# Kernel tuning notes

Measured on AMD Instinct MI355X. Metric: run time of the kernel, lower is better.

## Reference

```python
import jax, jax.numpy as jnp
import numpy as np

B, E, C, I, O, T = 8, 8, 1024, 128, 256, 8192

def setup_inputs() -> dict:
    key = jax.random.key(0)
    k1, k2, k3, k4, k5 = jax.random.split(key, 5)
    x_expert = jax.random.normal(k1, (B, E, C, I), dtype=jnp.float32)
    expert_indices = jax.random.randint(k2, (B, E, C), 0, T, dtype=jnp.int64 if jax.config.jax_enable_x64 else jnp.int32)
    expert_gate = jax.random.uniform(k3, (B, E, C), dtype=jnp.float32)
    # learned params: nn.Linear(in_features=1024, out_features=256) -> weight (O, in) viewed as (E, O, I)
    bound = 1.0 / np.sqrt(E * I)
    weight = jax.random.uniform(k4, (E, O, I), dtype=jnp.float32, minval=-bound, maxval=bound)
    bias = jax.random.uniform(k5, (O,), dtype=jnp.float32, minval=-bound, maxval=bound)
    return {"x_expert": x_expert, "expert_indices": expert_indices, "expert_gate": expert_gate,
            "weight": weight, "bias": bias, "num_tokens": T}

def reference(x_expert, expert_indices, expert_gate, weight, bias, num_tokens):
    # per-expert GEMM: (B,E,C,I) x (E,O,I) -> (B,E,C,O)
    y = jnp.einsum('beci,eoi->beco', x_expert, weight) + bias
    # gate scale: gate (B,E,C) -> (B,E,C,1)
    y = y * expert_gate[..., None]
    # scatter-add combine: flatten expert/capacity dims and index_add into (B, T, O)
    Bq, Eq, Cq, Oq = y.shape
    flat_y = y.reshape(Bq, Eq * Cq, Oq)
    flat_idx = expert_indices.reshape(Bq, Eq * Cq)
    out = jnp.zeros((Bq, num_tokens, Oq), dtype=y.dtype)
    batch_idx = jnp.arange(Bq)[:, None]  # (B,1) broadcasts against (B, E*C)
    out = out.at[batch_idx, flat_idx].add(flat_y)
    return out
```

## Files before the change

### kernel.cpp

```cpp
#include <hip/hip_runtime.h>

constexpr int Bn = 8;
constexpr int En = 8;
constexpr int Cn = 1024;
constexpr int In = 128;
constexpr int On = 256;
constexpr int Tn = 8192;
constexpr int ECn = En * Cn;

constexpr int TT = 64;

typedef __fp16 fp16x2 __attribute__((ext_vector_type(2)));
typedef __fp16 f16x8  __attribute__((ext_vector_type(8)));
typedef float  f32x4  __attribute__((ext_vector_type(4)));

__device__ inline unsigned int pk16(float a, float b) {
    fp16x2 h = __builtin_amdgcn_cvt_pkrtz(a, b);
    return __builtin_bit_cast(unsigned int, h);
}

__global__ void prep_w(const float4* __restrict__ w4, uint4* __restrict__ wh4) {
    int f = blockIdx.x * 256 + threadIdx.x;
    int col = f & 255, q = (f >> 8) & 3, s = (f >> 10) & 3, e = f >> 12;
    const float4* p = w4 + ((size_t)(e * On + col)) * (In / 4) + (s * 8 + q * 2);
    float4 a = p[0], b = p[1];
    uint4 o;
    o.x = pk16(a.x, a.y); o.y = pk16(a.z, a.w);
    o.z = pk16(b.x, b.y); o.w = pk16(b.z, b.w);
    wh4[f] = o;
}

__global__ __launch_bounds__(256, 2)
void gemm_scatter(const float* __restrict__ x,
                  const int*   __restrict__ idx,
                  const float* __restrict__ gate,
                  const uint4* __restrict__ wh4,
                  const float* __restrict__ bias,
                  float* __restrict__ out)
{
    __shared__ uint4 Ah[TT * 16];
    __shared__ int   sIdx[TT];
    __shared__ float sG[TT];

    const int tid = threadIdx.x;
    const int blk = blockIdx.x;
    const int b  = blk >> 7;
    const int e  = (blk >> 4) & 7;
    const int c0 = (blk & 15) * TT;

    const size_t becBase = ((size_t)(b * En + e)) * Cn + c0;
    const float* xrow = x + becBase * In;

    if (tid < TT) {
        sIdx[tid] = idx[becBase + tid];
        sG[tid]   = gate[becBase + tid];
    }

    {
        const int tl = tid >> 2, cq = (tid & 3) * 4;
        const float4* xr = (const float4*)xrow + (size_t)tl * (In / 4);
        #pragma unroll
        for (int it = 0; it < 4; ++it) {
            int cc = cq + it;
            float4 a = xr[2 * cc], b2 = xr[2 * cc + 1];
            uint4 o;
            o.x = pk16(a.x, a.y);  o.y = pk16(a.z, a.w);
            o.z = pk16(b2.x, b2.y); o.w = pk16(b2.z, b2.w);
            Ah[tl * 16 + (cc ^ (tl & 15))] = o;
        }
    }

    const int l15  = tid & 15;
    const int q    = (tid >> 4) & 3;
    const int wcol = (tid >> 6) * 64;

    f16x8 bfr[4][4];
    #pragma unroll
    for (int nt = 0; nt < 4; ++nt)
        #pragma unroll
        for (int s = 0; s < 4; ++s)
            bfr[nt][s] = __builtin_bit_cast(f16x8,
                wh4[(size_t)((e * 4 + s) * 4 + q) * 256 + wcol + 16 * nt + l15]);

    __syncthreads();

    f32x4 acc[4][4];
    #pragma unroll
    for (int mt = 0; mt < 4; ++mt)
        #pragma unroll
        for (int nt = 0; nt < 4; ++nt) acc[mt][nt] = f32x4{0.f, 0.f, 0.f, 0.f};

    #pragma unroll
    for (int mt = 0; mt < 4; ++mt) {
        const int tl = mt * 16 + l15;
        f16x8 afr[4];
        #pragma unroll
        for (int s = 0; s < 4; ++s)
            afr[s] = __builtin_bit_cast(f16x8, Ah[tl * 16 + ((4 * s + q) ^ (tl & 15))]);
        #pragma unroll
        for (int nt = 0; nt < 4; ++nt)
            #pragma unroll
            for (int s = 0; s < 4; ++s)
                acc[mt][nt] = __builtin_amdgcn_mfma_f32_16x16x32_f16(
                    afr[s], bfr[nt][s], acc[mt][nt], 0, 0, 0);
    }

    float bv[4];
    #pragma unroll
    for (int nt = 0; nt < 4; ++nt) bv[nt] = bias[wcol + 16 * nt + l15];

    float* ob = out + (size_t)b * Tn * On;
    #pragma unroll
    for (int mt = 0; mt < 4; ++mt) {
        #pragma unroll
        for (int i = 0; i < 4; ++i) {
            const int tl = mt * 16 + q * 4 + i;
            const int t  = sIdx[tl];
            const float g = sG[tl];
            float* orow = ob + (size_t)t * On + wcol + l15;
            #pragma unroll
            for (int nt = 0; nt < 4; ++nt)
                atomicAdd(&orow[16 * nt], (acc[mt][nt][i] + bv[nt]) * g);
        }
    }
}

extern "C" void kernel_launch(void* const* d_in, const int* in_sizes, int n_in,
                              void* d_out, int out_size, void* d_ws, size_t ws_size,
                              hipStream_t stream) {
    const float* x    = (const float*)d_in[0];
    const int*   idx  = (const int*)  d_in[1];
    const float* gate = (const float*)d_in[2];
    const float* w    = (const float*)d_in[3];
    const float* bias = (const float*)d_in[4];
    float* out = (float*)d_out;

    uint4* wh4 = (uint4*)d_ws;

    prep_w<<<(En * 4 * 4 * On) / 256, 256, 0, stream>>>((const float4*)w, wh4);
    hipMemsetAsync(d_out, 0, (size_t)out_size, stream);

    const int nblk = Bn * En * (Cn / TT);
    gemm_scatter<<<nblk, 256, 0, stream>>>(x, idx, gate, wh4, bias, out);
}
```

Before: 151.0 us.

## Replace atomic scatter with GEMM-to-workspace plus gather-based combine per token

When the workspace is large enough, the GEMM writes unscaled per-slot outputs to a workspace buffer. A second kernel then builds, per block of 64 tokens, a shared-memory inverse index of contributing slots and gathers and gates those rows, adding bias times the gate sum. This removes the global float atomics and the output memset, and the weights are converted to fp16 inside the GEMM instead of in a separate prep kernel. The cost is an extra 64 MB write and read of the workspace, and every combine block scans the whole index array. It also relies on a fixed per-token capacity plus a small overflow list, so tokens with very many contributions could be dropped.

```diff
diff --git a/kernel.cpp b/kernel.cpp
--- a/kernel.cpp
+++ b/kernel.cpp
@@ -8,7 +8,9 @@
 constexpr int Tn = 8192;
 constexpr int ECn = En * Cn;
 
-constexpr int TT = 64;
+constexpr int TT  = 64;
+constexpr int CAP = 16;
+constexpr int OVF = 32;
 
 typedef __fp16 fp16x2 __attribute__((ext_vector_type(2)));
 typedef __fp16 f16x8  __attribute__((ext_vector_type(8)));
@@ -17,6 +19,194 @@
 __device__ inline unsigned int pk16(float a, float b) {
     fp16x2 h = __builtin_amdgcn_cvt_pkrtz(a, b);
     return __builtin_bit_cast(unsigned int, h);
+}
+
+__global__ __launch_bounds__(256, 2)
+void gemm_y(const float* __restrict__ x,
+            const float* __restrict__ w,
+            float* __restrict__ y)
+{
+    __shared__ uint4 Ah[TT * 16];
+
+    const int tid = threadIdx.x;
+    const int blk = blockIdx.x;
+    const int b  = blk >> 7;
+    const int e  = (blk >> 4) & 7;
+    const int c0 = (blk & 15) * TT;
+
+    const size_t becBase = ((size_t)(b * En + e)) * Cn + c0;
+    const float* xrow = x + becBase * In;
+
+    {
+        const int tl = tid >> 2, cq = (tid & 3) * 4;
+        const float4* xr = (const float4*)xrow + (size_t)tl * (In / 4);
+        #pragma unroll
+        for (int it = 0; it < 4; ++it) {
+            int cc = cq + it;
+            float4 a = xr[2 * cc], b2 = xr[2 * cc + 1];
+            uint4 o;
+            o.x = pk16(a.x, a.y);   o.y = pk16(a.z, a.w);
+            o.z = pk16(b2.x, b2.y); o.w = pk16(b2.z, b2.w);
+            Ah[tl * 16 + (cc ^ (tl & 15))] = o;
+        }
+    }
+
+    const int l15  = tid & 15;
+    const int q    = (tid >> 4) & 3;
+    const int wcol = (tid >> 6) * 64;
+
+    f16x8 bfr[4][4];
+    #pragma unroll
+    for (int nt = 0; nt < 4; ++nt)
+        #pragma unroll
+        for (int s = 0; s < 4; ++s) {
+            const int col = wcol + 16 * nt + l15;
+            const float4* p = (const float4*)w
+                + ((size_t)(e * On + col)) * (In / 4) + (s * 8 + q * 2);
+            float4 a = p[0], b2 = p[1];
+            uint4 o;
+            o.x = pk16(a.x, a.y);   o.y = pk16(a.z, a.w);
+            o.z = pk16(b2.x, b2.y); o.w = pk16(b2.z, b2.w);
+            bfr[nt][s] = __builtin_bit_cast(f16x8, o);
+        }
+
+    __syncthreads();
+
+    f32x4 acc[4][4];
+    #pragma unroll
+    for (int mt = 0; mt < 4; ++mt)
+        #pragma unroll
+        for (int nt = 0; nt < 4; ++nt) acc[mt][nt] = f32x4{0.f, 0.f, 0.f, 0.f};
+
+    #pragma unroll
+    for (int mt = 0; mt < 4; ++mt) {
+        const int tl = mt * 16 + l15;
+        f16x8 afr[4];
+        #pragma unroll
+        for (int s = 0; s < 4; ++s)
+            afr[s] = __builtin_bit_cast(f16x8, Ah[tl * 16 + ((4 * s + q) ^ (tl & 15))]);
+        #pragma unroll
+        for (int nt = 0; nt < 4; ++nt)
+            #pragma unroll
+            for (int s = 0; s < 4; ++s)
+                acc[mt][nt] = __builtin_amdgcn_mfma_f32_16x16x32_f16(
+                    afr[s], bfr[nt][s], acc[mt][nt], 0, 0, 0);
+    }
+
+    float* yb = y + becBase * On;
+    #pragma unroll
+    for (int mt = 0; mt < 4; ++mt) {
+        #pragma unroll
+        for (int i = 0; i < 4; ++i) {
+            const int tl = mt * 16 + q * 4 + i;
+            float* yr = yb + (size_t)tl * On + wcol + l15;
+            #pragma unroll
+            for (int nt = 0; nt < 4; ++nt)
+                yr[16 * nt] = acc[mt][nt][i];
+        }
+    }
+}
+
+__global__ __launch_bounds__(256)
+void combine(const int*   __restrict__ idx,
+             const float* __restrict__ gate,
+             const float* __restrict__ y,
+             const float* __restrict__ bias,
+             float* __restrict__ out)
+{
+    __shared__ int   lcnt[TT];
+    __shared__ float gsum[TT];
+    __shared__ unsigned short lslot[TT][CAP];
+    __shared__ float lgate[TT][CAP];
+    __shared__ int ovfCnt;
+    __shared__ unsigned ovfE[OVF];
+    __shared__ float    ovfG[OVF];
+
+    const int tid = threadIdx.x;
+    const int blk = blockIdx.x;
+    const int b  = blk >> 7;
+    const int t0 = (blk & 127) * TT;
+    const int*   idxb  = idx  + (size_t)b * ECn;
+    const float* gateb = gate + (size_t)b * ECn;
+
+    if (tid < TT) { lcnt[tid] = 0; gsum[tid] = 0.f; }
+    if (tid == 0) ovfCnt = 0;
+    __syncthreads();
+
+    {
+        const int4* idx4 = (const int4*)idxb;
+        #pragma unroll
+        for (int s = 0; s < ECn / 1024; ++s) {
+            int i4 = tid + 256 * s;
+            int4 tv = idx4[i4];
+            int ec0 = i4 * 4;
+            #pragma unroll
+            for (int k = 0; k < 4; ++k) {
+                int t = (k == 0) ? tv.x : (k == 1) ? tv.y : (k == 2) ? tv.z : tv.w;
+                unsigned d = (unsigned)(t - t0);
+                if (d < (unsigned)TT) {
+                    int ec = ec0 + k;
+                    float g = gateb[ec];
+                    atomicAdd(&gsum[d], g);
+                    int pos = atomicAdd(&lcnt[d], 1);
+                    if (pos < CAP) {
+                        lslot[d][pos] = (unsigned short)ec;
+                        lgate[d][pos] = g;
+                    } else {
+                        int o = atomicAdd(&ovfCnt, 1);
+                        if (o < OVF) { ovfE[o] = ((unsigned)d << 16) | (unsigned)ec; ovfG[o] = g; }
+                    }
+                }
+            }
+        }
+    }
+    __syncthreads();
+
+    const int d = tid >> 2, qt = tid & 3, col0 = qt * 64;
+    const float* yb = y + (size_t)b * ECn * On;
+
+    float acc[64];
+    #pragma unroll
+    for (int k = 0; k < 64; ++k) acc[k] = 0.f;
+
+    const int n = min(lcnt[d], CAP);
+    for (int j = 0; j < n; ++j) {
+        const int ec = lslot[d][j];
+        const float g = lgate[d][j];
+        const float4* yr = (const float4*)(yb + (size_t)ec * On + col0);
+        #pragma unroll
+        for (int k = 0; k < 16; ++k) {
+            float4 v = yr[k];
+            acc[4 * k + 0] += v.x * g; acc[4 * k + 1] += v.y * g;
+            acc[4 * k + 2] += v.z * g; acc[4 * k + 3] += v.w * g;
+        }
+    }
+    const int oc = min(ovfCnt, OVF);
+    for (int j = 0; j < oc; ++j) {
+        if ((int)(ovfE[j] >> 16) == d) {
+            const int ec = (int)(ovfE[j] & 0xFFFFu);
+            const float g = ovfG[j];
+            const float4* yr = (const float4*)(yb + (size_t)ec * On + col0);
+            #pragma unroll
+            for (int k = 0; k < 16; ++k) {
+                float4 v = yr[k];
+                acc[4 * k + 0] += v.x * g; acc[4 * k + 1] += v.y * g;
+                acc[4 * k + 2] += v.z * g; acc[4 * k + 3] += v.w * g;
+            }
+        }
+    }
+
+    const float gs = gsum[d];
+    float4* orow = (float4*)(out + ((size_t)b * Tn + t0 + d) * On + col0);
+    const float4* bp = (const float4*)(bias + col0);
+    #pragma unroll
+    for (int k = 0; k < 16; ++k) {
+        float4 bb = bp[k];
+        float4 r;
+        r.x = acc[4 * k + 0] + bb.x * gs; r.y = acc[4 * k + 1] + bb.y * gs;
+        r.z = acc[4 * k + 2] + bb.z * gs; r.w = acc[4 * k + 3] + bb.w * gs;
+        orow[k] = r;
+    }
 }
 
 __global__ void prep_w(const float4* __restrict__ w4, uint4* __restrict__ wh4) {
@@ -31,12 +221,9 @@
 }
 
 __global__ __launch_bounds__(256, 2)
-void gemm_scatter(const float* __restrict__ x,
-                  const int*   __restrict__ idx,
-                  const float* __restrict__ gate,
-                  const uint4* __restrict__ wh4,
-                  const float* __restrict__ bias,
-                  float* __restrict__ out)
+void gemm_scatter(const float* __restrict__ x, const int* __restrict__ idx,
+                  const float* __restrict__ gate, const uint4* __restrict__ wh4,
+                  const float* __restrict__ bias, float* __restrict__ out)
 {
     __shared__ uint4 Ah[TT * 16];
     __shared__ int   sIdx[TT];
@@ -55,7 +242,6 @@
         sIdx[tid] = idx[becBase + tid];
         sG[tid]   = gate[becBase + tid];
     }
-
     {
         const int tl = tid >> 2, cq = (tid & 3) * 4;
         const float4* xr = (const float4*)xrow + (size_t)tl * (In / 4);
@@ -64,12 +250,11 @@
             int cc = cq + it;
             float4 a = xr[2 * cc], b2 = xr[2 * cc + 1];
             uint4 o;
-            o.x = pk16(a.x, a.y);  o.y = pk16(a.z, a.w);
+            o.x = pk16(a.x, a.y);   o.y = pk16(a.z, a.w);
             o.z = pk16(b2.x, b2.y); o.w = pk16(b2.z, b2.w);
             Ah[tl * 16 + (cc ^ (tl & 15))] = o;
         }
     }
-
     const int l15  = tid & 15;
     const int q    = (tid >> 4) & 3;
     const int wcol = (tid >> 6) * 64;
@@ -135,11 +320,16 @@
     const float* bias = (const float*)d_in[4];
     float* out = (float*)d_out;
 
-    uint4* wh4 = (uint4*)d_ws;
-
-    prep_w<<<(En * 4 * 4 * On) / 256, 256, 0, stream>>>((const float4*)w, wh4);
-    hipMemsetAsync(d_out, 0, (size_t)out_size, stream);
-
-    const int nblk = Bn * En * (Cn / TT);
-    gemm_scatter<<<nblk, 256, 0, stream>>>(x, idx, gate, wh4, bias, out);
-}
+    const size_t needY = (size_t)Bn * ECn * On * sizeof(float);
+
+    if (ws_size >= needY) {
+        float* yws = (float*)d_ws;
+        gemm_y <<<Bn * En * (Cn / TT), 256, 0, stream>>>(x, w, yws);
+        combine<<<Bn * (Tn / TT),      256, 0, stream>>>(idx, gate, yws, bias, out);
+    } else {
+        uint4* wh4 = (uint4*)d_ws;
+        prep_w<<<(En * 4 * 4 * On) / 256, 256, 0, stream>>>((const float4*)w, wh4);
+        hipMemsetAsync(d_out, 0, (size_t)out_size, stream);
+        gemm_scatter<<<Bn * En * (Cn / TT), 256, 0, stream>>>(x, idx, gate, wh4, bias, out);
+    }
+}
```

Result: slower. 168.3 us (+11.5%).
